# Kernel tuning notes

Hardware: AMD Instinct MI355X
Metric: run time of the kernel (lower is better)

Reference implementation:

```python
import jax, jax.numpy as jnp
import numpy as np

K_TOP = 64  # top-k selection size (init kwarg k)


def setup_inputs() -> dict:
    key = jax.random.key(0)
    k1, k2, k3, k4 = jax.random.split(key, 4)
    N, M, D = 512, 100000, 1024
    queries = jax.random.normal(k1, (N, D), dtype=jnp.float32)
    keys = jax.random.normal(k2, (M, D), dtype=jnp.float32)
    values = jax.random.normal(k3, (M, D), dtype=jnp.float32)
    affine = jax.random.normal(k4, (D,), dtype=jnp.float32)  # diag affine param (low_parameter=True)
    return {"queries": queries, "keys": keys, "values": values, "affine": affine}


def reference(queries, keys, values, affine):
    # low_parameter=True -> weight matrix is diag(affine): (queries @ diag(a)) == queries * a
    # scores[n, m] = (queries * affine) @ keys.T ; reduce max over queries dim (dim=0)
    scores = jnp.max(jnp.einsum('nd,md->nm', queries * affine, keys), axis=0)  # [M]
    weights, indices = jax.lax.top_k(scores, K_TOP)            # [k], [k]
    w = jax.nn.softmax(weights)                                # softmax over the k selected scores
    encoding = jnp.sum(w[:, None] * values[indices], axis=0)   # [V]
    return encoding, indices
```

## Files before the change

kernel.cpp:

```cpp
#include <hip/hip_runtime.h>
#include <cstdint>
#include <cstddef>


typedef __attribute__((ext_vector_type(8))) short bf16x8;
typedef __attribute__((ext_vector_type(4))) float f32x4;

static constexpr int NQ = 512;
static constexpr int DD = 1024;
static constexpr int MK = 100000;
static constexpr int BM = 128;
static constexpr int KSTEPS = DD / 64;
static constexpr int MBLK = (MK + BM - 1) / BM;
static constexpr int CAP = 1024;

static constexpr size_t QSTAGE_OFF   = 0;
static constexpr size_t QSTAGE_BYTES = (size_t)KSTEPS * 8 * NQ * 16;
static constexpr size_t SCORES_OFF   = QSTAGE_OFF + QSTAGE_BYTES;
static constexpr size_t SCORES_BYTES = (size_t)MBLK * BM * sizeof(float);
static constexpr size_t CIDX_OFF     = SCORES_OFF + SCORES_BYTES;
static constexpr size_t RESC_OFF     = CIDX_OFF + (size_t)CAP * 4;
static constexpr size_t CNT_OFF      = RESC_OFF + (size_t)CAP * 4;
static constexpr size_t HIST_OFF     = CNT_OFF + 64;
static constexpr size_t VLO_OFF      = HIST_OFF + 8192 * 4;

static constexpr int ABASE = 0;
static constexpr int BBASE = 32768;
static constexpr int GEMM_LDS = 32768 + 2 * 65536;

static __device__ __forceinline__ unsigned short f32_to_bf16_rne(float f) {
    unsigned int u = __float_as_uint(f);
    unsigned int r = (u + 0x7FFFu + ((u >> 16) & 1u)) >> 16;
    return (unsigned short)r;
}
static __device__ __forceinline__ unsigned int xform(float f) {
    unsigned int u = __float_as_uint(f);
    return u ^ ((unsigned int)((int)u >> 31) | 0x80000000u);
}
static __device__ __forceinline__ float unxform(unsigned int u) {
    unsigned int b = (u & 0x80000000u) ? (u ^ 0x80000000u) : ~u;
    return __uint_as_float(b);
}

typedef __attribute__((address_space(1))) const unsigned int g1u32;
typedef __attribute__((address_space(3))) unsigned int l3u32;
static __device__ __forceinline__ void async16(const void* g, void* l) {
    __builtin_amdgcn_global_load_lds((g1u32*)g, (l3u32*)(uintptr_t)l, 16, 0, 0);
}

__global__ void prep_q(const float* __restrict__ q, const float* __restrict__ a,
                       unsigned short* __restrict__ qs) {
    int id = blockIdx.x * 256 + threadIdx.x;
    int qq = id & 511;
    int j  = (id >> 9) & 7;
    int kk = id >> 12;
    int col = kk * 64 + (j >> 2) * 32 + (j & 3) * 8;

    const float* qrow = q + (size_t)qq * DD + col;
    float4 v0 = *(const float4*)(qrow);
    float4 v1 = *(const float4*)(qrow + 4);
    float4 a0 = *(const float4*)(a + col);
    float4 a1 = *(const float4*)(a + col + 4);
    float f[8] = {v0.x * a0.x, v0.y * a0.y, v0.z * a0.z, v0.w * a0.w,
                  v1.x * a1.x, v1.y * a1.y, v1.z * a1.z, v1.w * a1.w};
    bf16x8 o;
#pragma unroll
    for (int t = 0; t < 8; ++t) o[t] = (short)f32_to_bf16_rne(f[t]);
    *(bf16x8*)(qs + (size_t)id * 8) = o;
}

__launch_bounds__(512, 2)
__global__ void scores_gemm(const float* __restrict__ keys,
                            const unsigned short* __restrict__ qs,
                            float* __restrict__ scores) {
    extern __shared__ char smem[];
    const int tid  = threadIdx.x;
    const int wid  = tid >> 6;
    const int lane = tid & 63;
    const int g    = lane >> 4;
    const int r16  = lane & 15;
    const int wq   = wid & 3;
    const int wk   = wid >> 2;

    const int nwg = gridDim.x;
    const int qq8 = nwg >> 3, rr8 = nwg & 7;
    const int xcd = blockIdx.x & 7, loc = blockIdx.x >> 3;
    const int mb  = (xcd < rr8 ? xcd * (qq8 + 1) : rr8 * (qq8 + 1) + (xcd - rr8) * qq8) + loc;
    const int m0  = mb * BM;

    const int ar  = tid >> 2;
    const int c4  = (tid & 3) * 16;
    int garow = m0 + ar; if (garow >= MK) garow = MK - 1;
    const float* aptr = keys + (size_t)garow * DD + c4;
    const int as  = c4 >> 5;
    const int ag  = (c4 >> 3) & 3;
    const int aw0 = ((as * 4 + ag) * 128 + ar) * 16;

    const char* qsrc = (const char*)qs + (size_t)(64 * wid + lane) * 16;
    const int   bw0  = (64 * wid) * 16;

    f32x4 acc[4][8] = {};
    float4 P[4], Q[4];

#define STAGE_B(T1, BUF) do {                                                  \
    _Pragma("unroll")                                                          \
    for (int j = 0; j < 8; ++j)                                                \
        async16(qsrc + ((size_t)(T1) * 8 + j) * 8192,                          \
                smem + BBASE + (BUF) * 65536 + j * 8192 + bw0);                \
} while (0)

#define LOAD_A(TT, R) do {                                                     \
    int tA_ = (TT) < 15 ? (TT) : 15;                                           \
    _Pragma("unroll")                                                          \
    for (int i = 0; i < 4; ++i)                                                \
        R[i] = *(const float4*)(aptr + tA_ * 64 + i * 4);                      \
} while (0)

#define WRITE_A(R, BUF) do {                                                   \
    bf16x8 o0, o1;                                                             \
    _Pragma("unroll")                                                          \
    for (int i = 0; i < 4; ++i) {                                              \
        o0[i]     = (short)f32_to_bf16_rne(R[0][i]);                           \
        o0[i + 4] = (short)f32_to_bf16_rne(R[1][i]);                           \
        o1[i]     = (short)f32_to_bf16_rne(R[2][i]);                           \
        o1[i + 4] = (short)f32_to_bf16_rne(R[3][i]);                           \
    }                                                                          \
    *(bf16x8*)(smem + ABASE + (BUF) * 16384 + aw0)        = o0;                \
    *(bf16x8*)(smem + ABASE + (BUF) * 16384 + aw0 + 2048) = o1;                \
} while (0)

#define COMPUTE(BUF) do {                                                      \
    _Pragma("unroll")                                                          \
    for (int s = 0; s < 2; ++s) {                                              \
        bf16x8 af[4], bf[8];                                                   \
        _Pragma("unroll")                                                      \
        for (int rt = 0; rt < 4; ++rt)                                         \
            af[rt] = *(const bf16x8*)(smem + ABASE + (BUF) * 16384 +           \
                ((s * 4 + g) * 128 + wk * 64 + rt * 16 + r16) * 16);           \
        _Pragma("unroll")                                                      \
        for (int ct = 0; ct < 8; ++ct)                                         \
            bf[ct] = *(const bf16x8*)(smem + BBASE + (BUF) * 65536 +           \
                (s * 4 + g) * 8192 + (wq * 128 + ct * 16 + r16) * 16);         \
        __builtin_amdgcn_s_setprio(1);                                         \
        _Pragma("unroll")                                                      \
        for (int rt = 0; rt < 4; ++rt)                                         \
            _Pragma("unroll")                                                  \
            for (int ct = 0; ct < 8; ++ct)                                     \
                acc[rt][ct] = __builtin_amdgcn_mfma_f32_16x16x32_bf16(         \
                    af[rt], bf[ct], acc[rt][ct], 0, 0, 0);                     \
        __builtin_amdgcn_s_setprio(0);                                         \
    }                                                                          \
} while (0)

#define PIPE_BARRIER() do {                                                    \
    asm volatile("s_waitcnt vmcnt(4) lgkmcnt(0)" ::: "memory");                \
    __builtin_amdgcn_s_barrier();                                              \
    asm volatile("" ::: "memory");                                             \
} while (0)

#define ITER(T, RC, RL) do {                                                   \
    const int cur_ = (T) & 1, nxt_ = cur_ ^ 1;                                 \
    STAGE_B((T) + 1, nxt_);                                                    \
    asm volatile("" ::: "memory");       \
    LOAD_A((T) + 2, RL);                                                       \
    COMPUTE(cur_);                                                             \
    WRITE_A(RC, nxt_);                                                         \
    PIPE_BARRIER();                                                            \
} while (0)

    STAGE_B(0, 0);
    asm volatile("" ::: "memory");
    LOAD_A(0, P);
    LOAD_A(1, Q);
    WRITE_A(P, 0);
    PIPE_BARRIER();

    for (int t2 = 0; t2 < 7; ++t2) {
        ITER(2 * t2,     Q, P);
        ITER(2 * t2 + 1, P, Q);
    }
    ITER(14, Q, P);

    COMPUTE(1);
    __syncthreads();

#undef STAGE_B
#undef LOAD_A
#undef WRITE_A
#undef COMPUTE
#undef PIPE_BARRIER
#undef ITER

    float* wmax = (float*)smem;
#pragma unroll
    for (int rt = 0; rt < 4; ++rt) {
#pragma unroll
        for (int r = 0; r < 4; ++r) {
            float mx = acc[rt][0][r];
#pragma unroll
            for (int ct = 1; ct < 8; ++ct) mx = fmaxf(mx, acc[rt][ct][r]);
#pragma unroll
            for (int off = 1; off < 16; off <<= 1)
                mx = fmaxf(mx, __shfl_xor(mx, off));
            if (r16 == 0) wmax[wq * 128 + wk * 64 + rt * 16 + g * 4 + r] = mx;
        }
    }
    __syncthreads();
    if (tid < BM) {
        float mx = fmaxf(fmaxf(wmax[tid], wmax[128 + tid]),
                         fmaxf(wmax[256 + tid], wmax[384 + tid]));
        int gm = m0 + tid;
        if (gm < MK) scores[gm] = mx;
    }
}

__global__ void zero_hist(unsigned int* __restrict__ hist, int* __restrict__ cnt) {
    int i = blockIdx.x * 1024 + threadIdx.x;
    if (i < 8192) hist[i] = 0;
    if (i == 0) cnt[0] = 0;
}

__global__ void hist_build(const float* __restrict__ scores, unsigned int* __restrict__ hist) {
    __shared__ unsigned int lh[8192];
    for (int i = threadIdx.x; i < 8192; i += 256) lh[i] = 0;
    __syncthreads();
    for (int i = blockIdx.x * 256 + threadIdx.x; i < MK; i += gridDim.x * 256)
        atomicAdd(&lh[xform(scores[i]) >> 19], 1u);
    __syncthreads();
    for (int i = threadIdx.x; i < 8192; i += 256) {
        unsigned int c = lh[i];
        if (c) atomicAdd(&hist[i], c);
    }
}

__launch_bounds__(1024)
__global__ void find_thresh(const unsigned int* __restrict__ hist, float* __restrict__ vlo) {
    __shared__ unsigned int s0[1024], s1[1024];
    const int tid = threadIdx.x;
    unsigned int s = 0;
#pragma unroll
    for (int j = 0; j < 8; ++j) s += hist[tid * 8 + j];
    s0[tid] = s;
    __syncthreads();
    unsigned int* src = s0;
    unsigned int* dst = s1;
    for (int off = 1; off < 1024; off <<= 1) {
        unsigned int v = src[tid] + ((tid + off < 1024) ? src[tid + off] : 0u);
        __syncthreads();
        dst[tid] = v;
        __syncthreads();
        unsigned int* t = src; src = dst; dst = t;
    }
    unsigned int suf  = src[tid];
    unsigned int sufn = (tid < 1023) ? src[tid + 1] : 0u;
    if (suf >= 64u && sufn < 64u) {
        unsigned int acc = sufn;
        int b = tid * 8 + 7;
        for (;; --b) { acc += hist[b]; if (acc >= 64u) break; }
        vlo[0] = unxform(((unsigned int)b) << 19) - 1.0f;
    }
}

__global__ void collect(const float* __restrict__ scores, const float* __restrict__ vlo,
                        int* __restrict__ cidx, int* __restrict__ cnt) {
    const float t = vlo[0];
    for (int i = blockIdx.x * 256 + threadIdx.x; i < MK; i += gridDim.x * 256) {
        if (scores[i] >= t) {
            int p = atomicAdd(cnt, 1);
            if (p < CAP) cidx[p] = i;
        }
    }
}

__launch_bounds__(256)
__global__ void rescore(const float* __restrict__ q, const float* __restrict__ a,
                        const float* __restrict__ keys,
                        const int* __restrict__ cidx, const int* __restrict__ cnt,
                        float* __restrict__ resc) {
    __shared__ float w[1024];
    __shared__ float smax[4];
    const int b = blockIdx.x;
    if (b >= cnt[0]) return;
    const int m   = cidx[b];
    const int tid = threadIdx.x;

    for (int d = tid; d < 1024; d += 256) w[d] = a[d] * keys[(size_t)m * DD + d];
    __syncthreads();

    const int wid = tid >> 6, lane = tid & 63;
    float best = -__builtin_inff();
    for (int n = wid; n < NQ; n += 4) {
        const float* qr = q + (size_t)n * DD;
        float p = 0.f;
#pragma unroll
        for (int j = 0; j < 4; ++j) {
            float4 v  = *(const float4*)(qr + lane * 4 + 256 * j);
            float4 ww = *(const float4*)(&w[lane * 4 + 256 * j]);
            p += v.x * ww.x + v.y * ww.y + v.z * ww.z + v.w * ww.w;
        }
#pragma unroll
        for (int off = 1; off < 64; off <<= 1) p += __shfl_xor(p, off);
        best = fmaxf(best, p);
    }
    if (lane == 0) smax[wid] = best;
    __syncthreads();
    if (tid == 0)
        resc[b] = fmaxf(fmaxf(smax[0], smax[1]), fmaxf(smax[2], smax[3]));
}

__launch_bounds__(256)
__global__ void final_select(const int* __restrict__ cidx, const float* __restrict__ resc,
                             const int* __restrict__ cnt, const float* __restrict__ values,
                             float* __restrict__ out) {
    __shared__ float selw[64];
    __shared__ int   seli[64];
    const int tid = threadIdx.x;
    int nc = cnt[0];
    if (nc > CAP) nc = CAP;

    if (tid < 64) {
        const int lane = tid;
        float lv[16]; int li[16];
#pragma unroll
        for (int j = 0; j < 16; ++j) {
            int slot = lane + 64 * j;
            bool ok = slot < nc;
            lv[j] = ok ? resc[slot] : -__builtin_inff();
            li[j] = ok ? cidx[slot] : 0x7fffffff;
        }
        for (int it = 0; it < 64; ++it) {
            float bv = -__builtin_inff();
            int bg = 0x7fffffff, bj = 0;
#pragma unroll
            for (int j = 0; j < 16; ++j)
                if (lv[j] > bv || (lv[j] == bv && li[j] < bg)) { bv = lv[j]; bg = li[j]; bj = j; }
            int bcode = (lane << 4) | bj;
#pragma unroll
            for (int off = 1; off < 64; off <<= 1) {
                float ov = __shfl_xor(bv, off);
                int   og = __shfl_xor(bg, off);
                int   oc = __shfl_xor(bcode, off);
                if (ov > bv || (ov == bv && og < bg)) { bv = ov; bg = og; bcode = oc; }
            }
            if ((bcode >> 4) == lane) {
                int wj = bcode & 15;
#pragma unroll
                for (int j = 0; j < 16; ++j) if (j == wj) lv[j] = -__builtin_inff();
            }
            if (lane == 0) { selw[it] = bv; seli[it] = bg; }
        }
    }
    __syncthreads();

    if (tid < 64) {
        float x = selw[tid];
        float mx = x;
#pragma unroll
        for (int off = 1; off < 64; off <<= 1) mx = fmaxf(mx, __shfl_xor(mx, off));
        float e = expf(x - mx);
        float s = e;
#pragma unroll
        for (int off = 1; off < 64; off <<= 1) s += __shfl_xor(s, off);
        selw[tid] = e / s;
        out[DD + tid] = (float)seli[tid];
    }
    __syncthreads();

    for (int d = tid; d < DD; d += 256) {
        float accv = 0.f;
        for (int i = 0; i < 64; ++i)
            accv += selw[i] * values[(size_t)seli[i] * DD + d];
        out[d] = accv;
    }
}

extern "C" void kernel_launch(void* const* d_in, const int* in_sizes, int n_in,
                              void* d_out, int out_size, void* d_ws, size_t ws_size,
                              hipStream_t stream) {
    (void)in_sizes; (void)n_in; (void)out_size; (void)ws_size;
    const float* queries = (const float*)d_in[0];
    const float* keys    = (const float*)d_in[1];
    const float* values  = (const float*)d_in[2];
    const float* affine  = (const float*)d_in[3];
    float* out = (float*)d_out;
    char*  ws  = (char*)d_ws;

    unsigned short* qstage = (unsigned short*)(ws + QSTAGE_OFF);
    float* scores = (float*)(ws + SCORES_OFF);
    int*   cidx   = (int*)(ws + CIDX_OFF);
    float* resc   = (float*)(ws + RESC_OFF);
    int*   cnt    = (int*)(ws + CNT_OFF);
    unsigned int* hist = (unsigned int*)(ws + HIST_OFF);
    float* vlo    = (float*)(ws + VLO_OFF);

    hipFuncSetAttribute((const void*)scores_gemm,
                        hipFuncAttributeMaxDynamicSharedMemorySize, GEMM_LDS);

    prep_q<<<256, 256, 0, stream>>>(queries, affine, qstage);
    scores_gemm<<<MBLK, 512, GEMM_LDS, stream>>>(keys, qstage, scores);
    zero_hist<<<8, 1024, 0, stream>>>(hist, cnt);
    hist_build<<<64, 256, 0, stream>>>(scores, hist);
    find_thresh<<<1, 1024, 0, stream>>>(hist, vlo);
    collect<<<200, 256, 0, stream>>>(scores, vlo, cidx, cnt);
    rescore<<<CAP, 256, 0, stream>>>(queries, affine, keys, cidx, cnt, resc);
    final_select<<<1, 256, 0, stream>>>(cidx, resc, cnt, values, out);
}
```

Measured before the change: 445.0 us.

## Refine top-k threshold with two-level histogram and remap key loads

```diff
diff --git a/kernel.cpp b/kernel.cpp
--- a/kernel.cpp
+++ b/kernel.cpp
@@ -17,12 +17,14 @@
 static constexpr size_t QSTAGE_OFF   = 0;
 static constexpr size_t QSTAGE_BYTES = (size_t)KSTEPS * 8 * NQ * 16;
 static constexpr size_t SCORES_OFF   = QSTAGE_OFF + QSTAGE_BYTES;
-static constexpr size_t SCORES_BYTES = (size_t)MBLK * BM * sizeof(float);
+static constexpr size_t SCORES_BYTES = (size_t)MBLK * BM * 4;
 static constexpr size_t CIDX_OFF     = SCORES_OFF + SCORES_BYTES;
 static constexpr size_t RESC_OFF     = CIDX_OFF + (size_t)CAP * 4;
 static constexpr size_t CNT_OFF      = RESC_OFF + (size_t)CAP * 4;
-static constexpr size_t HIST_OFF     = CNT_OFF + 64;
-static constexpr size_t VLO_OFF      = HIST_OFF + 8192 * 4;
+static constexpr size_t HISTC_OFF    = CNT_OFF + 64;
+static constexpr size_t HISTF_OFF    = HISTC_OFF + 8192 * 4;
+static constexpr size_t TB_OFF       = HISTF_OFF + 8192 * 4;
+static constexpr size_t VLO_OFF      = TB_OFF + 64;
 
 static constexpr int ABASE = 0;
 static constexpr int BBASE = 32768;
@@ -88,13 +90,16 @@
     const int mb  = (xcd < rr8 ? xcd * (qq8 + 1) : rr8 * (qq8 + 1) + (xcd - rr8) * qq8) + loc;
     const int m0  = mb * BM;
 
-    const int ar  = tid >> 2;
-    const int c4  = (tid & 3) * 16;
-    int garow = m0 + ar; if (garow >= MK) garow = MK - 1;
-    const float* aptr = keys + (size_t)garow * DD + c4;
-    const int as  = c4 >> 5;
-    const int ag  = (c4 >> 3) & 3;
-    const int aw0 = ((as * 4 + ag) * 128 + ar) * 16;
+    const int c0 = (lane & 15) * 4;
+    const float* rowp[4];
+    int awb[4];
+#pragma unroll
+    for (int i = 0; i < 4; ++i) {
+        int rl = i * 32 + wid * 4 + (lane >> 4);
+        int gr = m0 + rl; if (gr > MK - 1) gr = MK - 1;
+        rowp[i] = keys + (size_t)gr * DD + c0;
+        awb[i] = (c0 >> 3) * 2048 + rl * 16 + (c0 & 4) * 2;
+    }
 
     const char* qsrc = (const char*)qs + (size_t)(64 * wid + lane) * 16;
     const int   bw0  = (64 * wid) * 16;
@@ -113,20 +118,19 @@
     int tA_ = (TT) < 15 ? (TT) : 15;                                           \
     _Pragma("unroll")                                                          \
     for (int i = 0; i < 4; ++i)                                                \
-        R[i] = *(const float4*)(aptr + tA_ * 64 + i * 4);                      \
+        R[i] = *(const float4*)(rowp[i] + tA_ * 64);                           \
 } while (0)
 
 #define WRITE_A(R, BUF) do {                                                   \
-    bf16x8 o0, o1;                                                             \
     _Pragma("unroll")                                                          \
     for (int i = 0; i < 4; ++i) {                                              \
-        o0[i]     = (short)f32_to_bf16_rne(R[0][i]);                           \
-        o0[i + 4] = (short)f32_to_bf16_rne(R[1][i]);                           \
-        o1[i]     = (short)f32_to_bf16_rne(R[2][i]);                           \
-        o1[i + 4] = (short)f32_to_bf16_rne(R[3][i]);                           \
+        unsigned long long pk_ =                                               \
+            (unsigned long long)f32_to_bf16_rne(R[i].x)                        \
+          | ((unsigned long long)f32_to_bf16_rne(R[i].y) << 16)                \
+          | ((unsigned long long)f32_to_bf16_rne(R[i].z) << 32)                \
+          | ((unsigned long long)f32_to_bf16_rne(R[i].w) << 48);               \
+        *(unsigned long long*)(smem + ABASE + (BUF) * 16384 + awb[i]) = pk_;   \
     }                                                                          \
-    *(bf16x8*)(smem + ABASE + (BUF) * 16384 + aw0)        = o0;                \
-    *(bf16x8*)(smem + ABASE + (BUF) * 16384 + aw0 + 2048) = o1;                \
 } while (0)
 
 #define COMPUTE(BUF) do {                                                      \
@@ -214,9 +218,10 @@
     }
 }
 
-__global__ void zero_hist(unsigned int* __restrict__ hist, int* __restrict__ cnt) {
+__global__ void zero_sel(unsigned int* __restrict__ hc, unsigned int* __restrict__ hf,
+                         int* __restrict__ cnt) {
     int i = blockIdx.x * 1024 + threadIdx.x;
-    if (i < 8192) hist[i] = 0;
+    if (i < 8192) { hc[i] = 0; hf[i] = 0; }
     if (i == 0) cnt[0] = 0;
 }
 
@@ -234,7 +239,7 @@
 }
 
 __launch_bounds__(1024)
-__global__ void find_thresh(const unsigned int* __restrict__ hist, float* __restrict__ vlo) {
+__global__ void find_coarse(const unsigned int* __restrict__ hist, int* __restrict__ tb) {
     __shared__ unsigned int s0[1024], s1[1024];
     const int tid = threadIdx.x;
     unsigned int s = 0;
@@ -254,10 +259,58 @@
     unsigned int suf  = src[tid];
     unsigned int sufn = (tid < 1023) ? src[tid + 1] : 0u;
     if (suf >= 64u && sufn < 64u) {
+        unsigned int acc = sufn, hb = 0;
+        int b = tid * 8 + 7;
+        for (;; --b) { hb = hist[b]; acc += hb; if (acc >= 64u) break; }
+        tb[0] = b;
+        tb[1] = (int)(acc - hb);
+    }
+}
+
+__global__ void hist_fine(const float* __restrict__ scores, const int* __restrict__ tb,
+                          unsigned int* __restrict__ fh) {
+    __shared__ unsigned int lh[8192];
+    for (int i = threadIdx.x; i < 8192; i += 256) lh[i] = 0;
+    __syncthreads();
+    const unsigned int b = (unsigned int)tb[0];
+    for (int i = blockIdx.x * 256 + threadIdx.x; i < MK; i += gridDim.x * 256) {
+        unsigned int u = xform(scores[i]);
+        if ((u >> 19) == b) atomicAdd(&lh[(u >> 6) & 8191u], 1u);
+    }
+    __syncthreads();
+    for (int i = threadIdx.x; i < 8192; i += 256) {
+        unsigned int c = lh[i];
+        if (c) atomicAdd(&fh[i], c);
+    }
+}
+
+__launch_bounds__(1024)
+__global__ void find_fine(const unsigned int* __restrict__ fh, const int* __restrict__ tb,
+                          float* __restrict__ vlo) {
+    __shared__ unsigned int s0[1024], s1[1024];
+    const int tid = threadIdx.x;
+    const unsigned int init = (unsigned int)tb[1];
+    unsigned int s = 0;
+#pragma unroll
+    for (int j = 0; j < 8; ++j) s += fh[tid * 8 + j];
+    s0[tid] = s;
+    __syncthreads();
+    unsigned int* src = s0;
+    unsigned int* dst = s1;
+    for (int off = 1; off < 1024; off <<= 1) {
+        unsigned int v = src[tid] + ((tid + off < 1024) ? src[tid + off] : 0u);
+        __syncthreads();
+        dst[tid] = v;
+        __syncthreads();
+        unsigned int* t = src; src = dst; dst = t;
+    }
+    unsigned int suf  = init + src[tid];
+    unsigned int sufn = init + ((tid < 1023) ? src[tid + 1] : 0u);
+    if (suf >= 64u && sufn < 64u) {
         unsigned int acc = sufn;
         int b = tid * 8 + 7;
-        for (;; --b) { acc += hist[b]; if (acc >= 64u) break; }
-        vlo[0] = unxform(((unsigned int)b) << 19) - 1.0f;
+        for (;; --b) { acc += fh[b]; if (acc >= 64u) break; }
+        vlo[0] = unxform(((unsigned int)tb[0] << 19) | ((unsigned int)b << 6)) - 0.8f;
     }
 }
 
@@ -277,14 +330,14 @@
                         const float* __restrict__ keys,
                         const int* __restrict__ cidx, const int* __restrict__ cnt,
                         float* __restrict__ resc) {
-    __shared__ float w[1024];
+    __shared__ float wsm[1024];
     __shared__ float smax[4];
     const int b = blockIdx.x;
     if (b >= cnt[0]) return;
     const int m   = cidx[b];
     const int tid = threadIdx.x;
 
-    for (int d = tid; d < 1024; d += 256) w[d] = a[d] * keys[(size_t)m * DD + d];
+    for (int d = tid; d < 1024; d += 256) wsm[d] = a[d] * keys[(size_t)m * DD + d];
     __syncthreads();
 
     const int wid = tid >> 6, lane = tid & 63;
@@ -295,7 +348,7 @@
 #pragma unroll
         for (int j = 0; j < 4; ++j) {
             float4 v  = *(const float4*)(qr + lane * 4 + 256 * j);
-            float4 ww = *(const float4*)(&w[lane * 4 + 256 * j]);
+            float4 ww = *(const float4*)(&wsm[lane * 4 + 256 * j]);
             p += v.x * ww.x + v.y * ww.y + v.z * ww.z + v.w * ww.w;
         }
 #pragma unroll
@@ -390,7 +443,9 @@
     int*   cidx   = (int*)(ws + CIDX_OFF);
     float* resc   = (float*)(ws + RESC_OFF);
     int*   cnt    = (int*)(ws + CNT_OFF);
-    unsigned int* hist = (unsigned int*)(ws + HIST_OFF);
+    unsigned int* hc = (unsigned int*)(ws + HISTC_OFF);
+    unsigned int* hf = (unsigned int*)(ws + HISTF_OFF);
+    int*   tb     = (int*)(ws + TB_OFF);
     float* vlo    = (float*)(ws + VLO_OFF);
 
     hipFuncSetAttribute((const void*)scores_gemm,
@@ -398,9 +453,11 @@
 
     prep_q<<<256, 256, 0, stream>>>(queries, affine, qstage);
     scores_gemm<<<MBLK, 512, GEMM_LDS, stream>>>(keys, qstage, scores);
-    zero_hist<<<8, 1024, 0, stream>>>(hist, cnt);
-    hist_build<<<64, 256, 0, stream>>>(scores, hist);
-    find_thresh<<<1, 1024, 0, stream>>>(hist, vlo);
+    zero_sel<<<8, 1024, 0, stream>>>(hc, hf, cnt);
+    hist_build<<<64, 256, 0, stream>>>(scores, hc);
+    find_coarse<<<1, 1024, 0, stream>>>(hc, tb);
+    hist_fine<<<64, 256, 0, stream>>>(scores, tb, hf);
+    find_fine<<<1, 1024, 0, stream>>>(hf, tb, vlo);
     collect<<<200, 256, 0, stream>>>(scores, vlo, cidx, cnt);
     rescore<<<CAP, 256, 0, stream>>>(queries, affine, keys, cidx, cnt, resc);
     final_select<<<1, 256, 0, stream>>>(cidx, resc, cnt, values, out);
```

Result: no change. 442.2 us (-0.6%).
